# Kernel optimization log

Measured on AMD Instinct MI355X. Metric: run time of the kernel, lower is better.

## Reference

```python
import jax, jax.numpy as jnp
import numpy as np

TOPK = 32  # module init arg


def setup_inputs() -> dict:
    key = jax.random.key(0)
    kq, kk, kv = jax.random.split(key, 3)
    B, T, S, H, E = 1, 2048, 2048, 16, 64
    return {
        "query": jax.random.normal(kq, (B, T, H, E), dtype=jnp.float32),
        "key": jax.random.normal(kk, (B, S, H, E), dtype=jnp.float32),
        "value": jax.random.normal(kv, (B, S, H, E), dtype=jnp.float32),
    }


def reference(query, key, value):
    B, T, H, E = query.shape
    S = key.shape[1]
    softmax_temp = 1.0 / np.sqrt(E)  # default: 1/sqrt(d_keys)
    topk = min(TOPK, S)

    q = query * jnp.asarray(softmax_temp, query.dtype)
    # full dense scores, as in the original module: [B, H, T, S]
    QK = jnp.einsum('bthe,bshe->bhts', q, key)

    # oracle top-k along keys; scatter True at top-k positions (exact mask semantics)
    _, topk_idx = jax.lax.top_k(QK, topk)  # [B, H, T, k]
    keep = jnp.put_along_axis(
        jnp.zeros(QK.shape, dtype=jnp.bool_), topk_idx, True, axis=-1,
        inplace=False,
    )
    QK = jnp.where(keep, QK, -jnp.inf)

    attn = jax.nn.softmax(QK, axis=-1)  # dropout p=0.0 -> identity
    output = jnp.einsum('bhts,bshd->bthd', attn, value)
    return output
```

## Files before the change

kernel.cpp:

```cpp
#include <hip/hip_runtime.h>
#include <stdint.h>


#define T_DIM 2048
#define S_DIM 2048
#define H_DIM 16
#define E_DIM 64
#define K_TOP 32
#define TT 8
#define NWAVE 8

typedef float v2f __attribute__((ext_vector_type(2)));

__device__ __forceinline__ v2f pk_fma(v2f a, v2f b, v2f c) {
    return __builtin_elementwise_fma(a, b, c);
}

__device__ __forceinline__ unsigned f2ord(float f) {
    unsigned b = __float_as_uint(f);
    return (b & 0x80000000u) ? ~b : (b | 0x80000000u);
}
__device__ __forceinline__ float ord2f(unsigned u) {
    unsigned b = (u & 0x80000000u) ? (u ^ 0x80000000u) : ~u;
    return __uint_as_float(b);
}

__global__ __launch_bounds__(256)
void transpose_k(const float* __restrict__ Kg, float* __restrict__ KT) {
    __shared__ float tile[64][65];
    const int tid = threadIdx.x;
    const int h   = blockIdx.x & (H_DIM - 1);
    const int sb  = (blockIdx.x >> 4) * 64;
    #pragma unroll
    for (int sw = 0; sw < 4; sw++) {
        int r = sw * 16 + (tid >> 4);
        int c = (tid & 15) * 4;
        float4 v = *(const float4*)(Kg + ((size_t)(sb + r) * H_DIM + h) * E_DIM + c);
        tile[r][c] = v.x; tile[r][c+1] = v.y; tile[r][c+2] = v.z; tile[r][c+3] = v.w;
    }
    __syncthreads();
    #pragma unroll
    for (int sw = 0; sw < 4; sw++) {
        int e = sw * 16 + (tid >> 4);
        int j = (tid & 15) * 4;
        float4 v = { tile[j][e], tile[j+1][e], tile[j+2][e], tile[j+3][e] };
        *(float4*)(KT + ((size_t)h * E_DIM + e) * S_DIM + sb + j) = v;
    }
}

__global__ __launch_bounds__(512, 2)
void topk_attn_kernel(const float* __restrict__ Qg,
                      const float* __restrict__ KT,
                      const float* __restrict__ Vg,
                      float* __restrict__ Out) {
    __shared__ __align__(16) unsigned short sU[TT][S_DIM];
    __shared__ unsigned candU[TT][64];
    __shared__ int      candI[TT][64];
    __shared__ unsigned wcnt[TT];
    __shared__ unsigned thrA[TT];

    const int tid  = threadIdx.x;
    const int lane = tid & 63;
    const int wv   = tid >> 6;
    const int bx   = blockIdx.x;
    const int h    = bx & (H_DIM - 1);
    const int tb   = bx >> 4;
    const int t0   = tb * TT;

    v2f acc2[TT][2];
    #pragma unroll
    for (int t = 0; t < TT; t++) { acc2[t][0] = (v2f)(0.f); acc2[t][1] = (v2f)(0.f); }

    const int   sb  = wv * 256 + (lane << 2);
    const float* kp = KT + (size_t)h * E_DIM * S_DIM + sb;
    const float* Qb = Qg + ((size_t)t0 * H_DIM + h) * E_DIM;

    float4 k0q = *(const float4*)(kp);
    float4 k1q = *(const float4*)(kp + S_DIM);
    for (int e2 = 0; e2 < 32; e2++) {
        const int ep = (e2 + 1) & 31;
        float4 n0q = *(const float4*)(kp + (size_t)(2 * ep)     * S_DIM);
        float4 n1q = *(const float4*)(kp + (size_t)(2 * ep + 1) * S_DIM);
        v2f k0lo = {k0q.x, k0q.y}, k0hi = {k0q.z, k0q.w};
        v2f k1lo = {k1q.x, k1q.y}, k1hi = {k1q.z, k1q.w};
        #pragma unroll
        for (int t = 0; t < TT; t++) {
            float2 qv = *(const float2*)(Qb + (size_t)t * (H_DIM * E_DIM) + 2 * e2);
            v2f qx = {qv.x, qv.x}, qy = {qv.y, qv.y};
            acc2[t][0] = pk_fma(qx, k0lo, acc2[t][0]);
            acc2[t][1] = pk_fma(qx, k0hi, acc2[t][1]);
            acc2[t][0] = pk_fma(qy, k1lo, acc2[t][0]);
            acc2[t][1] = pk_fma(qy, k1hi, acc2[t][1]);
        }
        k0q = n0q; k1q = n1q;
    }

    #pragma unroll
    for (int r = 0; r < TT; r++) {
        unsigned a = f2ord(acc2[r][0].x) >> 16;
        unsigned b = f2ord(acc2[r][0].y) >> 16;
        unsigned c = f2ord(acc2[r][1].x) >> 16;
        unsigned d = f2ord(acc2[r][1].y) >> 16;
        uint2 pk; pk.x = a | (b << 16); pk.y = c | (d << 16);
        *(uint2*)(&sU[r][sb]) = pk;
    }
    if (lane == 0) wcnt[wv] = 0u;
    __syncthreads();

    unsigned pk16[16];
    {
        const unsigned* rowp = (const unsigned*)(&sU[wv][0]);
        #pragma unroll
        for (int j = 0; j < 16; j++) pk16[j] = rowp[j * 64 + lane];
    }
    auto count16 = [&](unsigned t) -> int {
        int c = 0;
        #pragma unroll
        for (int j = 0; j < 16; j++) {
            c += __popcll(__ballot((pk16[j] & 0xFFFFu) >= t));
            c += __popcll(__ballot((pk16[j] >> 16) >= t));
        }
        return c;
    };

    unsigned thr = 0xC180u;
    int c = count16(thr);
    if (c < K_TOP || c > 64) {
        unsigned lo = (c >= K_TOP) ? thr : 0u;
        unsigned hi = (c >= K_TOP) ? 0x10000u : thr;
        bool found = false;
        while (!found && (hi - lo > 1u)) {
            unsigned mid = lo + ((hi - lo) >> 1);
            int cm = count16(mid);
            if (cm >= K_TOP && cm <= 64) { thr = mid; c = cm; found = true; }
            else if (cm >= K_TOP) lo = mid;
            else hi = mid;
        }
        if (!found) { thr = lo; c = count16(lo); }
    }
    if (lane == 0) thrA[wv] = thr;
    __syncthreads();

    #pragma unroll
    for (int r = 0; r < TT; r++) {
        unsigned tr = thrA[r];
        unsigned uu0 = f2ord(acc2[r][0].x);
        unsigned uu1 = f2ord(acc2[r][0].y);
        unsigned uu2 = f2ord(acc2[r][1].x);
        unsigned uu3 = f2ord(acc2[r][1].y);
        unsigned uu[4] = {uu0, uu1, uu2, uu3};
        #pragma unroll
        for (int q = 0; q < 4; q++) {
            if ((uu[q] >> 16) >= tr) {
                unsigned pos = atomicAdd(&wcnt[r], 1u);
                if (pos < 64u) {
                    candU[r][pos] = uu[q];
                    candI[r][pos] = sb + q;
                }
            }
        }
    }
    __syncthreads();

    unsigned nw = wcnt[wv];
    int n = (nw > 64u) ? 64 : (int)nw;

    unsigned long long key = 0ull;
    if (lane < n)
        key = (((unsigned long long)candU[wv][lane]) << 32)
            | (unsigned)(~candI[wv][lane]);
    #pragma unroll
    for (int k = 2; k <= 64; k <<= 1)
        #pragma unroll
        for (int j = k >> 1; j > 0; j >>= 1) {
            unsigned long long ok = __shfl_xor(key, j);
            bool takemax = ((lane & j) == 0) ^ ((lane & k) != 0);
            bool mineG   = key > ok;
            key = (takemax == mineG) ? key : ok;
        }

    const float* Vb = Vg + (size_t)h * E_DIM;
    float val  = ord2f((unsigned)(key >> 32)) * 0.125f;
    int   sidx = (int)(~(unsigned)key);
    float m = __shfl(val, 0);
    float w = (lane < K_TOP) ? expf(val - m) : 0.f;
    float Z = w;
    #pragma unroll
    for (int d = 32; d > 0; d >>= 1) Z += __shfl_xor(Z, d);
    float pr = w / Z;

    float o = 0.f;
    #pragma unroll
    for (int i2 = 0; i2 < K_TOP; i2++) {
        float pi = __shfl(pr, i2);
        int   s2 = __shfl(sidx, i2);
        o = fmaf(pi, Vb[(size_t)s2 * (H_DIM * E_DIM) + lane], o);
    }
    int t = t0 + wv;
    Out[((size_t)t * H_DIM + h) * E_DIM + lane] = o;
}

extern "C" void kernel_launch(void* const* d_in, const int* in_sizes, int n_in,
                              void* d_out, int out_size, void* d_ws, size_t ws_size,
                              hipStream_t stream) {
    const float* Q = (const float*)d_in[0];
    const float* K = (const float*)d_in[1];
    const float* V = (const float*)d_in[2];
    float* O  = (float*)d_out;
    float* KT = (float*)d_ws;
    (void)in_sizes; (void)n_in; (void)out_size; (void)ws_size;
    transpose_k<<<dim3(H_DIM * (S_DIM / 64)), dim3(256), 0, stream>>>(K, KT);
    topk_attn_kernel<<<dim3((T_DIM / TT) * H_DIM), dim3(512), 0, stream>>>(Q, KT, V, O);
}
```

Measured before the change: 217.1 us.

## Compute QK scores with split-bf16 MFMA and rescore candidates exactly in fp32

Replaces the FP32 packed-FMA score GEMM with bf16 MFMA, using a hi/lo split (three MFMAs per step) to approximate fp32 accuracy. K is pre-split into bf16 hi/lo arrays instead of being transposed. Rows per block go from 8 to 16 with a swizzled LDS score layout. The threshold is lowered slightly, the candidate cap is raised to 128, and candidates are rescored exactly in fp32 before a 128-wide bitonic sort. This moves the dominant dot-product work onto the matrix cores, at the cost of extra rescoring work, a larger sort, and some tie and precision risk in candidate selection.

```diff
diff --git a/kernel.cpp b/kernel.cpp
--- a/kernel.cpp
+++ b/kernel.cpp
@@ -7,14 +7,19 @@
 #define H_DIM 16
 #define E_DIM 64
 #define K_TOP 32
-#define TT 8
-#define NWAVE 8
-
-typedef float v2f __attribute__((ext_vector_type(2)));
-
-__device__ __forceinline__ v2f pk_fma(v2f a, v2f b, v2f c) {
-    return __builtin_elementwise_fma(a, b, c);
-}
+#define TT 16
+#define CAND_CAP 128
+
+typedef float f32x4 __attribute__((ext_vector_type(4)));
+typedef short bf16x4 __attribute__((ext_vector_type(4)));
+typedef short bf16x8 __attribute__((ext_vector_type(8)));
+
+#if __has_builtin(__builtin_amdgcn_mfma_f32_16x16x16bf16_1k)
+#define HAVE_MFMA16 1
+#define MFMA16(a,b,c) __builtin_amdgcn_mfma_f32_16x16x16bf16_1k((a),(b),(c),0,0,0)
+#else
+#define HAVE_MFMA16 0
+#endif
 
 __device__ __forceinline__ unsigned f2ord(float f) {
     unsigned b = __float_as_uint(f);
@@ -24,38 +29,39 @@
     unsigned b = (u & 0x80000000u) ? (u ^ 0x80000000u) : ~u;
     return __uint_as_float(b);
 }
+__device__ __forceinline__ unsigned short bf16rne(float f) {
+    unsigned u = __float_as_uint(f);
+    unsigned r = u + 0x7FFFu + ((u >> 16) & 1u);
+    return (unsigned short)(r >> 16);
+}
+__device__ __forceinline__ float bf2f(unsigned short h) {
+    return __uint_as_float(((unsigned)h) << 16);
+}
 
 __global__ __launch_bounds__(256)
-void transpose_k(const float* __restrict__ Kg, float* __restrict__ KT) {
-    __shared__ float tile[64][65];
-    const int tid = threadIdx.x;
-    const int h   = blockIdx.x & (H_DIM - 1);
-    const int sb  = (blockIdx.x >> 4) * 64;
-    #pragma unroll
-    for (int sw = 0; sw < 4; sw++) {
-        int r = sw * 16 + (tid >> 4);
-        int c = (tid & 15) * 4;
-        float4 v = *(const float4*)(Kg + ((size_t)(sb + r) * H_DIM + h) * E_DIM + c);
-        tile[r][c] = v.x; tile[r][c+1] = v.y; tile[r][c+2] = v.z; tile[r][c+3] = v.w;
-    }
-    __syncthreads();
-    #pragma unroll
-    for (int sw = 0; sw < 4; sw++) {
-        int e = sw * 16 + (tid >> 4);
-        int j = (tid & 15) * 4;
-        float4 v = { tile[j][e], tile[j+1][e], tile[j+2][e], tile[j+3][e] };
-        *(float4*)(KT + ((size_t)h * E_DIM + e) * S_DIM + sb + j) = v;
-    }
-}
-
-__global__ __launch_bounds__(512, 2)
+void prep_k(const float* __restrict__ Kg,
+            unsigned short* __restrict__ Khi,
+            unsigned short* __restrict__ Klo) {
+    const size_t base = (size_t)blockIdx.x * 1024 + threadIdx.x * 4;
+    float4 v = *(const float4*)(Kg + base);
+    ushort4 hh, ll;
+    hh.x = bf16rne(v.x); ll.x = bf16rne(v.x - bf2f(hh.x));
+    hh.y = bf16rne(v.y); ll.y = bf16rne(v.y - bf2f(hh.y));
+    hh.z = bf16rne(v.z); ll.z = bf16rne(v.z - bf2f(hh.z));
+    hh.w = bf16rne(v.w); ll.w = bf16rne(v.w - bf2f(hh.w));
+    *(ushort4*)(Khi + base) = hh;
+    *(ushort4*)(Klo + base) = ll;
+}
+
+__global__ __launch_bounds__(512, 4)
 void topk_attn_kernel(const float* __restrict__ Qg,
-                      const float* __restrict__ KT,
+                      const float* __restrict__ Kg,
                       const float* __restrict__ Vg,
+                      const unsigned short* __restrict__ Khi,
+                      const unsigned short* __restrict__ Klo,
                       float* __restrict__ Out) {
     __shared__ __align__(16) unsigned short sU[TT][S_DIM];
-    __shared__ unsigned candU[TT][64];
-    __shared__ int      candI[TT][64];
+    __shared__ int      candI[TT][CAND_CAP];
     __shared__ unsigned wcnt[TT];
     __shared__ unsigned thrA[TT];
 
@@ -64,140 +70,201 @@
     const int wv   = tid >> 6;
     const int bx   = blockIdx.x;
     const int h    = bx & (H_DIM - 1);
-    const int tb   = bx >> 4;
-    const int t0   = tb * TT;
-
-    v2f acc2[TT][2];
-    #pragma unroll
-    for (int t = 0; t < TT; t++) { acc2[t][0] = (v2f)(0.f); acc2[t][1] = (v2f)(0.f); }
-
-    const int   sb  = wv * 256 + (lane << 2);
-    const float* kp = KT + (size_t)h * E_DIM * S_DIM + sb;
-    const float* Qb = Qg + ((size_t)t0 * H_DIM + h) * E_DIM;
-
-    float4 k0q = *(const float4*)(kp);
-    float4 k1q = *(const float4*)(kp + S_DIM);
-    for (int e2 = 0; e2 < 32; e2++) {
-        const int ep = (e2 + 1) & 31;
-        float4 n0q = *(const float4*)(kp + (size_t)(2 * ep)     * S_DIM);
-        float4 n1q = *(const float4*)(kp + (size_t)(2 * ep + 1) * S_DIM);
-        v2f k0lo = {k0q.x, k0q.y}, k0hi = {k0q.z, k0q.w};
-        v2f k1lo = {k1q.x, k1q.y}, k1hi = {k1q.z, k1q.w};
-        #pragma unroll
-        for (int t = 0; t < TT; t++) {
-            float2 qv = *(const float2*)(Qb + (size_t)t * (H_DIM * E_DIM) + 2 * e2);
-            v2f qx = {qv.x, qv.x}, qy = {qv.y, qv.y};
-            acc2[t][0] = pk_fma(qx, k0lo, acc2[t][0]);
-            acc2[t][1] = pk_fma(qx, k0hi, acc2[t][1]);
-            acc2[t][0] = pk_fma(qy, k1lo, acc2[t][0]);
-            acc2[t][1] = pk_fma(qy, k1hi, acc2[t][1]);
-        }
-        k0q = n0q; k1q = n1q;
-    }
+    const int t0   = (bx >> 4) * TT;
+    if (tid < TT) wcnt[tid] = 0u;
+
+    const int am = lane & 15;
+    const int ag = lane >> 4;
+
+    const float* Qrow = Qg + ((size_t)(t0 + am) * H_DIM + h) * E_DIM;
+#if HAVE_MFMA16
+    bf16x4 Ahi[4], Alo[4];
+    #pragma unroll
+    for (int ks = 0; ks < 4; ks++) {
+        #pragma unroll
+        for (int i = 0; i < 4; i++) {
+            float q = Qrow[ks * 16 + ag * 4 + i];
+            unsigned short hi = bf16rne(q);
+            Ahi[ks][i] = (short)hi;
+            Alo[ks][i] = (short)bf16rne(q - bf2f(hi));
+        }
+    }
+#else
+    bf16x8 Ahi[2], Alo[2];
+    #pragma unroll
+    for (int ks = 0; ks < 2; ks++) {
+        #pragma unroll
+        for (int i = 0; i < 8; i++) {
+            float q = Qrow[ks * 32 + (ag << 3) + i];
+            unsigned short hi = bf16rne(q);
+            Ahi[ks][i] = (short)hi;
+            Alo[ks][i] = (short)bf16rne(q - bf2f(hi));
+        }
+    }
+#endif
+
+    f32x4 acc[16];
+    #pragma unroll
+    for (int j = 0; j < 16; j++) acc[j] = (f32x4)(0.f);
+
+    const int sw = wv * 256;
+    const size_t bbase = ((size_t)(sw + am) * H_DIM + h) * E_DIM;
+    #pragma unroll
+    for (int j = 0; j < 16; j++) {
+        const size_t off = bbase + (size_t)j * (16 * H_DIM * E_DIM);
+#if HAVE_MFMA16
+        #pragma unroll
+        for (int ks = 0; ks < 4; ks++) {
+            bf16x4 bh = *(const bf16x4*)(Khi + off + ks * 16 + ag * 4);
+            bf16x4 bl = *(const bf16x4*)(Klo + off + ks * 16 + ag * 4);
+            acc[j] = MFMA16(Ahi[ks], bh, acc[j]);
+            acc[j] = MFMA16(Ahi[ks], bl, acc[j]);
+            acc[j] = MFMA16(Alo[ks], bh, acc[j]);
+        }
+#else
+        #pragma unroll
+        for (int ks = 0; ks < 2; ks++) {
+            bf16x8 bh = *(const bf16x8*)(Khi + off + ks * 32 + (ag << 3));
+            bf16x8 bl = *(const bf16x8*)(Klo + off + ks * 32 + (ag << 3));
+            acc[j] = __builtin_amdgcn_mfma_f32_16x16x32_bf16(Ahi[ks], bh, acc[j], 0, 0, 0);
+            acc[j] = __builtin_amdgcn_mfma_f32_16x16x32_bf16(Ahi[ks], bl, acc[j], 0, 0, 0);
+            acc[j] = __builtin_amdgcn_mfma_f32_16x16x32_bf16(Alo[ks], bh, acc[j], 0, 0, 0);
+        }
+#endif
+    }
+
+    #pragma unroll
+    for (int j = 0; j < 16; j++) {
+        const int cswz = (sw + j * 16 + am) ^ (ag << 4);
+        #pragma unroll
+        for (int i = 0; i < 4; i++)
+            sU[ag * 4 + i][cswz] = (unsigned short)(f2ord(acc[j][i]) >> 16);
+    }
+    __syncthreads();
+
+    #pragma unroll
+    for (int rr = 0; rr < 2; rr++) {
+        const int r = wv * 2 + rr;
+        const unsigned* rowp = (const unsigned*)(&sU[r][0]);
+        unsigned pk16[16];
+        #pragma unroll
+        for (int jj = 0; jj < 16; jj++) pk16[jj] = rowp[jj * 64 + lane];
+        auto count16 = [&](unsigned t) -> int {
+            int c = 0;
+            #pragma unroll
+            for (int jj = 0; jj < 16; jj++) {
+                c += __popcll(__ballot((pk16[jj] & 0xFFFFu) >= t));
+                c += __popcll(__ballot((pk16[jj] >> 16) >= t));
+            }
+            return c;
+        };
+        unsigned thr = 0xC180u;
+        int c = count16(thr);
+        if (c < K_TOP || c > 64) {
+            unsigned lo = (c >= K_TOP) ? thr : 0u;
+            unsigned hi = (c >= K_TOP) ? 0x10000u : thr;
+            bool found = false;
+            while (!found && (hi - lo > 1u)) {
+                unsigned mid = lo + ((hi - lo) >> 1);
+                int cm = count16(mid);
+                if (cm >= K_TOP && cm <= 64) { thr = mid; found = true; }
+                else if (cm >= K_TOP) lo = mid;
+                else hi = mid;
+            }
+            if (!found) thr = lo;
+        }
+        if (lane == 0) thrA[r] = (thr > 3u) ? (thr - 3u) : 1u;
+    }
+    __syncthreads();
 
     #pragma unroll
     for (int r = 0; r < TT; r++) {
-        unsigned a = f2ord(acc2[r][0].x) >> 16;
-        unsigned b = f2ord(acc2[r][0].y) >> 16;
-        unsigned c = f2ord(acc2[r][1].x) >> 16;
-        unsigned d = f2ord(acc2[r][1].y) >> 16;
-        uint2 pk; pk.x = a | (b << 16); pk.y = c | (d << 16);
-        *(uint2*)(&sU[r][sb]) = pk;
-    }
-    if (lane == 0) wcnt[wv] = 0u;
+        const unsigned tr = thrA[r];
+        const unsigned sz = ((unsigned)(r >> 2) & 3u) << 4;
+        const unsigned* rowp = (const unsigned*)(&sU[r][0]);
+        #pragma unroll
+        for (int half = 0; half < 2; half++) {
+            const int c32 = (sw >> 1) + half * 64 + lane;
+            const unsigned w = rowp[c32];
+            if ((w & 0xFFFFu) >= tr) {
+                unsigned p = atomicAdd(&wcnt[r], 1u);
+                if (p < CAND_CAP) candI[r][p] = (int)((unsigned)(2 * c32) ^ sz);
+            }
+            if ((w >> 16) >= tr) {
+                unsigned p = atomicAdd(&wcnt[r], 1u);
+                if (p < CAND_CAP) candI[r][p] = (int)((unsigned)(2 * c32 + 1) ^ sz);
+            }
+        }
+    }
     __syncthreads();
 
-    unsigned pk16[16];
-    {
-        const unsigned* rowp = (const unsigned*)(&sU[wv][0]);
-        #pragma unroll
-        for (int j = 0; j < 16; j++) pk16[j] = rowp[j * 64 + lane];
-    }
-    auto count16 = [&](unsigned t) -> int {
-        int c = 0;
-        #pragma unroll
-        for (int j = 0; j < 16; j++) {
-            c += __popcll(__ballot((pk16[j] & 0xFFFFu) >= t));
-            c += __popcll(__ballot((pk16[j] >> 16) >= t));
-        }
-        return c;
-    };
-
-    unsigned thr = 0xC180u;
-    int c = count16(thr);
-    if (c < K_TOP || c > 64) {
-        unsigned lo = (c >= K_TOP) ? thr : 0u;
-        unsigned hi = (c >= K_TOP) ? 0x10000u : thr;
-        bool found = false;
-        while (!found && (hi - lo > 1u)) {
-            unsigned mid = lo + ((hi - lo) >> 1);
-            int cm = count16(mid);
-            if (cm >= K_TOP && cm <= 64) { thr = mid; c = cm; found = true; }
-            else if (cm >= K_TOP) lo = mid;
-            else hi = mid;
-        }
-        if (!found) { thr = lo; c = count16(lo); }
-    }
-    if (lane == 0) thrA[wv] = thr;
-    __syncthreads();
-
-    #pragma unroll
-    for (int r = 0; r < TT; r++) {
-        unsigned tr = thrA[r];
-        unsigned uu0 = f2ord(acc2[r][0].x);
-        unsigned uu1 = f2ord(acc2[r][0].y);
-        unsigned uu2 = f2ord(acc2[r][1].x);
-        unsigned uu3 = f2ord(acc2[r][1].y);
-        unsigned uu[4] = {uu0, uu1, uu2, uu3};
-        #pragma unroll
-        for (int q = 0; q < 4; q++) {
-            if ((uu[q] >> 16) >= tr) {
-                unsigned pos = atomicAdd(&wcnt[r], 1u);
-                if (pos < 64u) {
-                    candU[r][pos] = uu[q];
-                    candI[r][pos] = sb + q;
+    for (int rr = 0; rr < 2; rr++) {
+        const int r = wv * 2 + rr;
+        const int t = t0 + r;
+        const unsigned nw = wcnt[r];
+        const int n = (nw > CAND_CAP) ? CAND_CAP : (int)nw;
+        const float* Qr = Qg + ((size_t)t * H_DIM + h) * E_DIM;
+
+        const int s0 = (lane < n) ? candI[r][lane] : -1;
+        const int s1 = (lane + 64 < n) ? candI[r][lane + 64] : -1;
+        unsigned long long key0 = 0ull, key1 = 0ull;
+        {
+            const float* k0p = Kg + ((size_t)(s0 < 0 ? 0 : s0) * H_DIM + h) * E_DIM;
+            const float* k1p = Kg + ((size_t)(s1 < 0 ? 0 : s1) * H_DIM + h) * E_DIM;
+            float a0 = 0.f, a1 = 0.f;
+            #pragma unroll
+            for (int e4 = 0; e4 < 16; e4++) {
+                float4 q4 = *(const float4*)(Qr + e4 * 4);
+                float4 k04 = *(const float4*)(k0p + e4 * 4);
+                float4 k14 = *(const float4*)(k1p + e4 * 4);
+                a0 = fmaf(q4.x, k04.x, a0); a1 = fmaf(q4.x, k14.x, a1);
+                a0 = fmaf(q4.y, k04.y, a0); a1 = fmaf(q4.y, k14.y, a1);
+                a0 = fmaf(q4.z, k04.z, a0); a1 = fmaf(q4.z, k14.z, a1);
+                a0 = fmaf(q4.w, k04.w, a0); a1 = fmaf(q4.w, k14.w, a1);
+            }
+            if (s0 >= 0) key0 = (((unsigned long long)f2ord(a0)) << 32) | (unsigned)(~s0);
+            if (s1 >= 0) key1 = (((unsigned long long)f2ord(a1)) << 32) | (unsigned)(~s1);
+        }
+
+        #pragma unroll
+        for (int k = 2; k <= 128; k <<= 1) {
+            #pragma unroll
+            for (int j = k >> 1; j > 0; j >>= 1) {
+                if (j == 64) {
+                    unsigned long long mx = key0 > key1 ? key0 : key1;
+                    unsigned long long mn = key0 > key1 ? key1 : key0;
+                    key0 = mx; key1 = mn;
+                } else {
+                    unsigned long long o0 = __shfl_xor(key0, j);
+                    unsigned long long o1 = __shfl_xor(key1, j);
+                    const bool lj  = (lane & j) == 0;
+                    const bool tm0 = lj ^ ((lane & k) != 0);
+                    const bool tm1 = lj ^ (((lane + 64) & k) != 0);
+                    key0 = (tm0 == (key0 > o0)) ? key0 : o0;
+                    key1 = (tm1 == (key1 > o1)) ? key1 : o1;
                 }
             }
         }
-    }
-    __syncthreads();
-
-    unsigned nw = wcnt[wv];
-    int n = (nw > 64u) ? 64 : (int)nw;
-
-    unsigned long long key = 0ull;
-    if (lane < n)
-        key = (((unsigned long long)candU[wv][lane]) << 32)
-            | (unsigned)(~candI[wv][lane]);
-    #pragma unroll
-    for (int k = 2; k <= 64; k <<= 1)
-        #pragma unroll
-        for (int j = k >> 1; j > 0; j >>= 1) {
-            unsigned long long ok = __shfl_xor(key, j);
-            bool takemax = ((lane & j) == 0) ^ ((lane & k) != 0);
-            bool mineG   = key > ok;
-            key = (takemax == mineG) ? key : ok;
-        }
-
-    const float* Vb = Vg + (size_t)h * E_DIM;
-    float val  = ord2f((unsigned)(key >> 32)) * 0.125f;
-    int   sidx = (int)(~(unsigned)key);
-    float m = __shfl(val, 0);
-    float w = (lane < K_TOP) ? expf(val - m) : 0.f;
-    float Z = w;
-    #pragma unroll
-    for (int d = 32; d > 0; d >>= 1) Z += __shfl_xor(Z, d);
-    float pr = w / Z;
-
-    float o = 0.f;
-    #pragma unroll
-    for (int i2 = 0; i2 < K_TOP; i2++) {
-        float pi = __shfl(pr, i2);
-        int   s2 = __shfl(sidx, i2);
-        o = fmaf(pi, Vb[(size_t)s2 * (H_DIM * E_DIM) + lane], o);
-    }
-    int t = t0 + wv;
-    Out[((size_t)t * H_DIM + h) * E_DIM + lane] = o;
+
+        float val  = ord2f((unsigned)(key0 >> 32)) * 0.125f;
+        int   sidx = (int)(~(unsigned)key0);
+        float m = __shfl(val, 0);
+        float w = (lane < K_TOP) ? expf(val - m) : 0.f;
+        float Z = w;
+        #pragma unroll
+        for (int d = 32; d > 0; d >>= 1) Z += __shfl_xor(Z, d);
+        float pr = w / Z;
+
+        const float* Vb = Vg + (size_t)h * E_DIM;
+        float o = 0.f;
+        #pragma unroll
+        for (int i2 = 0; i2 < K_TOP; i2++) {
+            float pi = __shfl(pr, i2);
+            int   s2 = __shfl(sidx, i2);
+            o = fmaf(pi, Vb[(size_t)s2 * (H_DIM * E_DIM) + lane], o);
+        }
+        Out[((size_t)t * H_DIM + h) * E_DIM + lane] = o;
+    }
 }
 
 extern "C" void kernel_launch(void* const* d_in, const int* in_sizes, int n_in,
@@ -206,9 +273,10 @@
     const float* Q = (const float*)d_in[0];
     const float* K = (const float*)d_in[1];
     const float* V = (const float*)d_in[2];
-    float* O  = (float*)d_out;
-    float* KT = (float*)d_ws;
+    float* O = (float*)d_out;
+    unsigned short* Khi = (unsigned short*)d_ws;
+    unsigned short* Klo = Khi + (size_t)S_DIM * H_DIM * E_DIM;
     (void)in_sizes; (void)n_in; (void)out_size; (void)ws_size;
-    transpose_k<<<dim3(H_DIM * (S_DIM / 64)), dim3(256), 0, stream>>>(K, KT);
-    topk_attn_kernel<<<dim3((T_DIM / TT) * H_DIM), dim3(512), 0, stream>>>(Q, KT, V, O);
-}
+    prep_k<<<dim3(S_DIM * H_DIM * E_DIM / 1024), dim3(256), 0, stream>>>(K, Khi, Klo);
+    topk_attn_kernel<<<dim3((T_DIM / TT) * H_DIM), dim3(512), 0, stream>>>(Q, K, V, Khi, Klo, O);
+}
```

Measured after the change: 553.6 us. 2.55x slower.
